# Kernel tuning notes

Measured on AMD Instinct MI355X. Metric: run time of the kernel, lower is better.

Reference implementation:

```python
import jax, jax.numpy as jnp
import numpy as np

B, ES, HS, NL, NOUT, T = 16384, 64, 64, 3, 2, 128


def setup_inputs() -> dict:
    key = jax.random.key(0)
    ks = jax.random.split(key, 9)
    k = 1.0 / np.sqrt(HS)
    u = lambda kk, shape: jax.random.uniform(kk, shape, jnp.float32, -k, k)
    return {
        "agentFutureTrajEnc": jax.random.normal(ks[0], (B, ES), jnp.float32),
        "emb_w": u(ks[1], (ES, ES)),
        "emb_b": u(ks[2], (ES,)),
        "w_ih": u(ks[3], (NL, 3 * HS, ES)),
        "w_hh": u(ks[4], (NL, 3 * HS, HS)),
        "b_ih": u(ks[5], (NL, 3 * HS)),
        "b_hh": u(ks[6], (NL, 3 * HS)),
        "out_w": u(ks[7], (NOUT, HS)),
        "out_b": u(ks[8], (NOUT,)),
        "target_length": T,
        "batch_size": B,
    }


def _gru_cell(x, h, Wi, Wh, bi, bh):
    # PyTorch GRU cell math: gates ordered (r, z, n)
    gi = x @ Wi.T + bi            # (B, 3*hs)
    gh = h @ Wh.T + bh            # (B, 3*hs)
    ir, iz, inn = jnp.split(gi, 3, axis=-1)
    hr, hz, hn = jnp.split(gh, 3, axis=-1)
    r = jax.nn.sigmoid(ir + hr)
    z = jax.nn.sigmoid(iz + hz)
    n = jnp.tanh(inn + r * hn)
    return (1.0 - z) * n + z * h


def reference(agentFutureTrajEnc, emb_w, emb_b, w_ih, w_hh, b_ih, b_hh, out_w, out_b,
              target_length, batch_size):
    nl = w_ih.shape[0]
    # hidden initialized by repeating the encoding across layers: (nl, B, hs)
    h0 = jnp.broadcast_to(agentFutureTrajEnc[None], (nl,) + agentFutureTrajEnc.shape)

    def step(carry, _):
        x, h = carry                      # x: (B, es), h: (nl, B, hs)
        inp = x @ emb_w.T + emb_b         # embedding Linear(es->es)
        new_h = []
        for l in range(nl):               # small fixed layer loop
            hl = _gru_cell(inp, h[l], w_ih[l], w_hh[l], b_ih[l], b_hh[l])
            new_h.append(hl)
            inp = hl
        h = jnp.stack(new_h)              # (nl, B, hs)
        out = inp @ out_w.T + out_b       # (B, nout)
        return (h[-1], h), out            # next input is top-layer hidden

    _, outs = jax.lax.scan(step, (agentFutureTrajEnc, h0), None, length=target_length)
    return jnp.transpose(outs, (1, 0, 2))  # (B, T, nout)
```

## Files before the change

### kernel.cpp

```cpp
#include <hip/hip_runtime.h>


#define ESZ   64
#define HSZ   64
#define TLEN  128
#define NOUTC 2
#define LDW   72
#define TB    (16*LDW)
#define L2E   1.44269504f

typedef _Float16 half8 __attribute__((ext_vector_type(8)));
typedef _Float16 half4 __attribute__((ext_vector_type(4)));
typedef float    floatx4 __attribute__((ext_vector_type(4)));
typedef float    floatx2 __attribute__((ext_vector_type(2)));

#define MFMA(a, b, c) __builtin_amdgcn_mfma_f32_16x16x32_f16((a), (b), (c), 0, 0, 0)

__global__ __launch_bounds__(768, 3) void gru_pipe(
    const float* __restrict__ enc,
    const float* __restrict__ emb_w,
    const float* __restrict__ emb_b,
    const float* __restrict__ w_ih,
    const float* __restrict__ w_hh,
    const float* __restrict__ b_ih,
    const float* __restrict__ b_hh,
    const float* __restrict__ out_w,
    const float* __restrict__ out_b,
    float* __restrict__ out)
{
    __shared__ _Float16 s_hl[3 * 4 * 2 * TB];
    __shared__ float    s_btmp[3 * 64];
    __shared__ int      s_flag[12];

    const int tid  = threadIdx.x;
    const int wave = tid >> 6, lane = tid & 63;
    const int l = wave >> 2, g = wave & 3;
    const int q = lane >> 4, c = lane & 15;
    const int u  = (g << 4) | c;
    const int u4 = (g << 4) | (q << 2);
    const long wgbase = (long)blockIdx.x * 64;

    if (tid < 512) {
        const int row = tid >> 3, k0 = (tid & 7) << 3;
        const int j = row >> 4, rr = row & 15;
        const float* p = enc + (wgbase + row) * ESZ + k0;
        floatx4 s0 = *(const floatx4*)p;
        floatx4 s1 = *(const floatx4*)(p + 4);
        half8 v;
        #pragma unroll
        for (int x = 0; x < 4; ++x) { v[x] = (_Float16)s0[x]; v[4 + x] = (_Float16)s1[x]; }
        #pragma unroll
        for (int ly = 0; ly < 3; ++ly)
            *(half8*)&s_hl[((ly * 4 + j) * 2 + 1) * TB + rr * LDW + k0] = v;
    }
    if (tid < 12) s_flag[tid] = 0;

    auto ldw8s = [&](const float* p, float sc) {
        floatx4 a = *(const floatx4*)p, b = *(const floatx4*)(p + 4);
        half8 v;
        #pragma unroll
        for (int x = 0; x < 4; ++x) { v[x] = (_Float16)(a[x] * sc); v[4 + x] = (_Float16)(b[x] * sc); }
        return v;
    };
    half8 fR[4], fZ[4], fNi[2], fNh[2], fO[2];
    fO[0] = fO[1] = half8{};
    if (l == 0) {
        const float* wi = w_ih;
        const float* wh = w_hh;
        floatx4 aR[4], aZ[4], aN[4];
        #pragma unroll
        for (int x = 0; x < 4; ++x) { aR[x] = {0,0,0,0}; aZ[x] = {0,0,0,0}; aN[x] = {0,0,0,0}; }
        float bR = 0.f, bZ = 0.f, bN = 0.f;
        for (int k4 = 0; k4 < 64; k4 += 4) {
            floatx4 wr4 = *(const floatx4*)(wi + (u) * 64 + k4);
            floatx4 wz4 = *(const floatx4*)(wi + (64 + u) * 64 + k4);
            floatx4 wn4 = *(const floatx4*)(wi + (128 + u) * 64 + k4);
            floatx4 be4 = *(const floatx4*)(emb_b + k4);
            #pragma unroll
            for (int kk = 0; kk < 4; ++kk) {
                const float* er = emb_w + (k4 + kk) * 64;
                floatx4 e0 = *(const floatx4*)(er + q * 8);
                floatx4 e1 = *(const floatx4*)(er + q * 8 + 4);
                floatx4 e2 = *(const floatx4*)(er + 32 + q * 8);
                floatx4 e3 = *(const floatx4*)(er + 32 + q * 8 + 4);
                const float wr = wr4[kk], wz = wz4[kk], wn = wn4[kk];
                aR[0] += wr * e0; aR[1] += wr * e1; aR[2] += wr * e2; aR[3] += wr * e3;
                aZ[0] += wz * e0; aZ[1] += wz * e1; aZ[2] += wz * e2; aZ[3] += wz * e3;
                aN[0] += wn * e0; aN[1] += wn * e1; aN[2] += wn * e2; aN[3] += wn * e3;
                bR += wr * be4[kk]; bZ += wz * be4[kk]; bN += wn * be4[kk];
            }
        }
        #pragma unroll
        for (int x = 0; x < 4; ++x) {
            fR[0][x] = (_Float16)(-L2E * aR[0][x]);   fR[0][4 + x] = (_Float16)(-L2E * aR[1][x]);
            fR[1][x] = (_Float16)(-L2E * aR[2][x]);   fR[1][4 + x] = (_Float16)(-L2E * aR[3][x]);
            fZ[0][x] = (_Float16)(-L2E * aZ[0][x]);   fZ[0][4 + x] = (_Float16)(-L2E * aZ[1][x]);
            fZ[1][x] = (_Float16)(-L2E * aZ[2][x]);   fZ[1][4 + x] = (_Float16)(-L2E * aZ[3][x]);
            fNi[0][x] = (_Float16)(2*L2E * aN[0][x]); fNi[0][4 + x] = (_Float16)(2*L2E * aN[1][x]);
            fNi[1][x] = (_Float16)(2*L2E * aN[2][x]); fNi[1][4 + x] = (_Float16)(2*L2E * aN[3][x]);
        }
        fR[2]  = ldw8s(wh + (u) * 64 + q * 8, -L2E);        fR[3]  = ldw8s(wh + (u) * 64 + 32 + q * 8, -L2E);
        fZ[2]  = ldw8s(wh + (64 + u) * 64 + q * 8, -L2E);   fZ[3]  = ldw8s(wh + (64 + u) * 64 + 32 + q * 8, -L2E);
        fNh[0] = ldw8s(wh + (128 + u) * 64 + q * 8, 2*L2E); fNh[1] = ldw8s(wh + (128 + u) * 64 + 32 + q * 8, 2*L2E);
        if (q == 0) {
            s_btmp[u] = bR; s_btmp[64 + u] = bZ; s_btmp[128 + u] = bN;
        }
        const int oc = (c < NOUTC) ? c : 0;
        fO[0] = ldw8s(out_w + oc * 64 + q * 8, 1.f);
        fO[1] = ldw8s(out_w + oc * 64 + 32 + q * 8, 1.f);
    } else {
        const float* wi = w_ih + l * 3 * HSZ * ESZ;
        const float* wh = w_hh + l * 3 * HSZ * ESZ;
        fR[0]  = ldw8s(wi + (u) * 64 + q * 8, -L2E);        fR[1]  = ldw8s(wi + (u) * 64 + 32 + q * 8, -L2E);
        fR[2]  = ldw8s(wh + (u) * 64 + q * 8, -L2E);        fR[3]  = ldw8s(wh + (u) * 64 + 32 + q * 8, -L2E);
        fZ[0]  = ldw8s(wi + (64 + u) * 64 + q * 8, -L2E);   fZ[1]  = ldw8s(wi + (64 + u) * 64 + 32 + q * 8, -L2E);
        fZ[2]  = ldw8s(wh + (64 + u) * 64 + q * 8, -L2E);   fZ[3]  = ldw8s(wh + (64 + u) * 64 + 32 + q * 8, -L2E);
        fNi[0] = ldw8s(wi + (128 + u) * 64 + q * 8, 2*L2E); fNi[1] = ldw8s(wi + (128 + u) * 64 + 32 + q * 8, 2*L2E);
        fNh[0] = ldw8s(wh + (128 + u) * 64 + q * 8, 2*L2E); fNh[1] = ldw8s(wh + (128 + u) * 64 + 32 + q * 8, 2*L2E);
    }
    __syncthreads();

    floatx4 bR4, bZ4, bNi4, bNh4;
    if (l == 0) {
        #pragma unroll
        for (int i = 0; i < 4; ++i) {
            bR4[i]  = -L2E * (s_btmp[u4 + i] + b_ih[u4 + i] + b_hh[u4 + i]);
            bZ4[i]  = -L2E * (s_btmp[64 + u4 + i] + b_ih[64 + u4 + i] + b_hh[64 + u4 + i]);
            bNi4[i] = 2.f * L2E * (s_btmp[128 + u4 + i] + b_ih[128 + u4 + i]);
            bNh4[i] = 2.f * L2E * b_hh[128 + u4 + i];
        }
    } else {
        const int b0 = l * 192;
        floatx4 bi0 = *(const floatx4*)(b_ih + b0 + u4),       bh0 = *(const floatx4*)(b_hh + b0 + u4);
        floatx4 bi1 = *(const floatx4*)(b_ih + b0 + 64 + u4),  bh1 = *(const floatx4*)(b_hh + b0 + 64 + u4);
        floatx4 bi2 = *(const floatx4*)(b_ih + b0 + 128 + u4), bh2 = *(const floatx4*)(b_hh + b0 + 128 + u4);
        #pragma unroll
        for (int i = 0; i < 4; ++i) {
            bR4[i]  = -L2E * (bi0[i] + bh0[i]);
            bZ4[i]  = -L2E * (bi1[i] + bh1[i]);
            bNi4[i] = 2.f * L2E * bi2[i];
            bNh4[i] = 2.f * L2E * bh2[i];
        }
    }
    const float ob0 = out_b[0], ob1 = out_b[1];

    floatx4 ca0 = *(const floatx4*)(enc + (wgbase + 0 * 16 + c) * 64 + u4);
    floatx4 ca1 = *(const floatx4*)(enc + (wgbase + 1 * 16 + c) * 64 + u4);
    floatx4 ca2 = *(const floatx4*)(enc + (wgbase + 2 * 16 + c) * 64 + u4);
    floatx4 ca3 = *(const floatx4*)(enc + (wgbase + 3 * 16 + c) * 64 + u4);

    const int ar = c * LDW + (q << 3);
    const int fh = l * 4, fx = ((l == 0) ? 2 : (l - 1)) * 4;

    auto iter = [&](const int j, floatx4& carr, const int t) {
        const int parh = (t + 1) & 1, parw = t & 1;
        { volatile const int* f = &s_flag[fh + j]; const int tg = 4 * t; while (*f < tg) {} }
        asm volatile("" ::: "memory");
        const _Float16* hb = s_hl + ((fh + j) * 2 + parh) * TB;
        half8 ah0 = *(const half8*)(hb + ar), ah1 = *(const half8*)(hb + ar + 32);
        floatx4 accr = bR4, accz = bZ4, accni = bNi4, accnh = bNh4;
        accr  = MFMA(fR[2], ah0, accr);   accr  = MFMA(fR[3], ah1, accr);
        accz  = MFMA(fZ[2], ah0, accz);   accz  = MFMA(fZ[3], ah1, accz);
        accnh = MFMA(fNh[0], ah0, accnh); accnh = MFMA(fNh[1], ah1, accnh);
        { volatile const int* f = &s_flag[fx + j]; const int tg = (l == 0) ? 4 * t : 4 * t + 4; while (*f < tg) {} }
        asm volatile("" ::: "memory");
        const _Float16* xb = (l == 0) ? s_hl + ((2 * 4 + j) * 2 + parh) * TB
                                      : s_hl + (((l - 1) * 4 + j) * 2 + parw) * TB;
        half8 bx0 = *(const half8*)(xb + ar), bx1 = *(const half8*)(xb + ar + 32);
        if (l == 0 && g == 0 && t >= 1) {
            floatx4 oa = {ob0, ob1, 0.f, 0.f};
            oa = MFMA(fO[0], bx0, oa);
            oa = MFMA(fO[1], bx1, oa);
            if (q == 0) {
                const long row = wgbase + j * 16 + c;
                *(floatx2*)(out + (row * TLEN + (t - 1)) * NOUTC) = floatx2{oa[0], oa[1]};
            }
        }
        accr  = MFMA(fR[0], bx0, accr);   accr  = MFMA(fR[1], bx1, accr);
        accz  = MFMA(fZ[0], bx0, accz);   accz  = MFMA(fZ[1], bx1, accz);
        accni = MFMA(fNi[0], bx0, accni); accni = MFMA(fNi[1], bx1, accni);
        half4 hv4; floatx4 hnew;
        #pragma unroll
        for (int i = 0; i < 4; ++i) {
            const float r  = __builtin_amdgcn_rcpf(1.f + __builtin_amdgcn_exp2f(accr[i]));
            const float z  = __builtin_amdgcn_rcpf(1.f + __builtin_amdgcn_exp2f(accz[i]));
            const float a  = accni[i] + r * accnh[i];
            const float n  = 1.f - 2.f * __builtin_amdgcn_rcpf(1.f + __builtin_amdgcn_exp2f(a));
            const float hv = n + z * (carr[i] - n);
            hnew[i] = hv; hv4[i] = (_Float16)hv;
        }
        *(half4*)(s_hl + ((fh + j) * 2 + parw) * TB + c * LDW + u4) = hv4;
        carr = hnew;
        asm volatile("s_waitcnt lgkmcnt(0)" ::: "memory");
        if (lane == 0) atomicAdd(&s_flag[fh + j], 1);
    };

    for (int t = 0; t < TLEN; ++t) {
        iter(0, ca0, t); iter(1, ca1, t); iter(2, ca2, t); iter(3, ca3, t);
    }

    if (l == 0 && g == 0) {
        #pragma unroll
        for (int j = 0; j < 4; ++j) {
            { volatile const int* f = &s_flag[2 * 4 + j]; while (*f < 4 * TLEN) {} }
            asm volatile("" ::: "memory");
            const _Float16* xb = s_hl + ((2 * 4 + j) * 2 + 1) * TB;
            half8 bx0 = *(const half8*)(xb + ar), bx1 = *(const half8*)(xb + ar + 32);
            floatx4 oa = {ob0, ob1, 0.f, 0.f};
            oa = MFMA(fO[0], bx0, oa);
            oa = MFMA(fO[1], bx1, oa);
            if (q == 0) {
                const long row = wgbase + j * 16 + c;
                *(floatx2*)(out + (row * TLEN + 127) * NOUTC) = floatx2{oa[0], oa[1]};
            }
        }
    }
}

extern "C" void kernel_launch(void* const* d_in, const int* in_sizes, int n_in,
                              void* d_out, int out_size, void* d_ws, size_t ws_size,
                              hipStream_t stream) {
    (void)in_sizes; (void)n_in; (void)d_ws; (void)ws_size; (void)out_size;
    const int grid = 16384 / 64;
    gru_pipe<<<grid, 768, 0, stream>>>(
        (const float*)d_in[0],
        (const float*)d_in[1],
        (const float*)d_in[2],
        (const float*)d_in[3],
        (const float*)d_in[4],
        (const float*)d_in[5],
        (const float*)d_in[6],
        (const float*)d_in[7],
        (const float*)d_in[8],
        (float*)d_out);
}
```

Measured before the change: 448.3 us.

## Process 32-row batch tiles per pipeline stage and spread output projection across waves

Changes the per-workgroup pipeline from four 16-row tiles to two 32-row tiles. Each wave now issues twice as many independent MFMAs per flag wait, which halves the number of spin-wait and atomic synchronisation points per timestep. The output projection moves out of the critical path: instead of layer-0 wave 0 computing it before its gate MFMAs, it is spread across the four layer-0 waves and issued after the flag release. The cost is higher register pressure and coarser pipeline granularity, which reduces overlap between layers.

```diff
diff --git a/kernel.cpp b/kernel.cpp
--- a/kernel.cpp
+++ b/kernel.cpp
@@ -5,8 +5,9 @@
 #define HSZ   64
 #define TLEN  128
 #define NOUTC 2
+#define NT    2
 #define LDW   72
-#define TB    (16*LDW)
+#define TB32  (32*LDW)
 #define L2E   1.44269504f
 
 typedef _Float16 half8 __attribute__((ext_vector_type(8)));
@@ -28,9 +29,9 @@
     const float* __restrict__ out_b,
     float* __restrict__ out)
 {
-    __shared__ _Float16 s_hl[3 * 4 * 2 * TB];
+    __shared__ _Float16 s_hl[3 * NT * 2 * TB32];
     __shared__ float    s_btmp[3 * 64];
-    __shared__ int      s_flag[12];
+    __shared__ int      s_flag[3 * NT];
 
     const int tid  = threadIdx.x;
     const int wave = tid >> 6, lane = tid & 63;
@@ -42,7 +43,7 @@
 
     if (tid < 512) {
         const int row = tid >> 3, k0 = (tid & 7) << 3;
-        const int j = row >> 4, rr = row & 15;
+        const int j = row >> 5, rr = row & 31;
         const float* p = enc + (wgbase + row) * ESZ + k0;
         floatx4 s0 = *(const floatx4*)p;
         floatx4 s1 = *(const floatx4*)(p + 4);
@@ -51,9 +52,9 @@
         for (int x = 0; x < 4; ++x) { v[x] = (_Float16)s0[x]; v[4 + x] = (_Float16)s1[x]; }
         #pragma unroll
         for (int ly = 0; ly < 3; ++ly)
-            *(half8*)&s_hl[((ly * 4 + j) * 2 + 1) * TB + rr * LDW + k0] = v;
-    }
-    if (tid < 12) s_flag[tid] = 0;
+            *(half8*)&s_hl[((ly * NT + j) * 2 + 1) * TB32 + rr * LDW + k0] = v;
+    }
+    if (tid < 3 * NT) s_flag[tid] = 0;
 
     auto ldw8s = [&](const float* p, float sc) {
         floatx4 a = *(const floatx4*)p, b = *(const floatx4*)(p + 4);
@@ -144,75 +145,107 @@
     }
     const float ob0 = out_b[0], ob1 = out_b[1];
 
-    floatx4 ca0 = *(const floatx4*)(enc + (wgbase + 0 * 16 + c) * 64 + u4);
-    floatx4 ca1 = *(const floatx4*)(enc + (wgbase + 1 * 16 + c) * 64 + u4);
-    floatx4 ca2 = *(const floatx4*)(enc + (wgbase + 2 * 16 + c) * 64 + u4);
-    floatx4 ca3 = *(const floatx4*)(enc + (wgbase + 3 * 16 + c) * 64 + u4);
+    floatx4 ca00 = *(const floatx4*)(enc + (wgbase +  0 + c) * 64 + u4);
+    floatx4 ca01 = *(const floatx4*)(enc + (wgbase + 16 + c) * 64 + u4);
+    floatx4 ca10 = *(const floatx4*)(enc + (wgbase + 32 + c) * 64 + u4);
+    floatx4 ca11 = *(const floatx4*)(enc + (wgbase + 48 + c) * 64 + u4);
 
     const int ar = c * LDW + (q << 3);
-    const int fh = l * 4, fx = ((l == 0) ? 2 : (l - 1)) * 4;
-
-    auto iter = [&](const int j, floatx4& carr, const int t) {
-        const int parh = (t + 1) & 1, parw = t & 1;
+    const int fh = l * NT, fx = ((l == 0) ? 2 : (l - 1)) * NT;
+    const int myj = g >> 1, mys = g & 1;
+
+    auto iter = [&](const int j, floatx4& cs0, floatx4& cs1, const int t,
+                    const int parh, const int parw) {
         { volatile const int* f = &s_flag[fh + j]; const int tg = 4 * t; while (*f < tg) {} }
         asm volatile("" ::: "memory");
-        const _Float16* hb = s_hl + ((fh + j) * 2 + parh) * TB;
-        half8 ah0 = *(const half8*)(hb + ar), ah1 = *(const half8*)(hb + ar + 32);
-        floatx4 accr = bR4, accz = bZ4, accni = bNi4, accnh = bNh4;
-        accr  = MFMA(fR[2], ah0, accr);   accr  = MFMA(fR[3], ah1, accr);
-        accz  = MFMA(fZ[2], ah0, accz);   accz  = MFMA(fZ[3], ah1, accz);
-        accnh = MFMA(fNh[0], ah0, accnh); accnh = MFMA(fNh[1], ah1, accnh);
+        const _Float16* hb = s_hl + ((fh + j) * 2 + parh) * TB32;
+        half8 ah00 = *(const half8*)(hb + ar),             ah01 = *(const half8*)(hb + ar + 32);
+        half8 ah10 = *(const half8*)(hb + ar + 16 * LDW),  ah11 = *(const half8*)(hb + ar + 16 * LDW + 32);
+        floatx4 accr0 = bR4, accz0 = bZ4, accnh0 = bNh4;
+        floatx4 accr1 = bR4, accz1 = bZ4, accnh1 = bNh4;
+        accr0  = MFMA(fR[2], ah00, accr0);   accr0  = MFMA(fR[3], ah01, accr0);
+        accz0  = MFMA(fZ[2], ah00, accz0);   accz0  = MFMA(fZ[3], ah01, accz0);
+        accnh0 = MFMA(fNh[0], ah00, accnh0); accnh0 = MFMA(fNh[1], ah01, accnh0);
+        accr1  = MFMA(fR[2], ah10, accr1);   accr1  = MFMA(fR[3], ah11, accr1);
+        accz1  = MFMA(fZ[2], ah10, accz1);   accz1  = MFMA(fZ[3], ah11, accz1);
+        accnh1 = MFMA(fNh[0], ah10, accnh1); accnh1 = MFMA(fNh[1], ah11, accnh1);
         { volatile const int* f = &s_flag[fx + j]; const int tg = (l == 0) ? 4 * t : 4 * t + 4; while (*f < tg) {} }
         asm volatile("" ::: "memory");
-        const _Float16* xb = (l == 0) ? s_hl + ((2 * 4 + j) * 2 + parh) * TB
-                                      : s_hl + (((l - 1) * 4 + j) * 2 + parw) * TB;
-        half8 bx0 = *(const half8*)(xb + ar), bx1 = *(const half8*)(xb + ar + 32);
-        if (l == 0 && g == 0 && t >= 1) {
-            floatx4 oa = {ob0, ob1, 0.f, 0.f};
-            oa = MFMA(fO[0], bx0, oa);
-            oa = MFMA(fO[1], bx1, oa);
-            if (q == 0) {
-                const long row = wgbase + j * 16 + c;
-                *(floatx2*)(out + (row * TLEN + (t - 1)) * NOUTC) = floatx2{oa[0], oa[1]};
-            }
-        }
-        accr  = MFMA(fR[0], bx0, accr);   accr  = MFMA(fR[1], bx1, accr);
-        accz  = MFMA(fZ[0], bx0, accz);   accz  = MFMA(fZ[1], bx1, accz);
-        accni = MFMA(fNi[0], bx0, accni); accni = MFMA(fNi[1], bx1, accni);
-        half4 hv4; floatx4 hnew;
-        #pragma unroll
-        for (int i = 0; i < 4; ++i) {
-            const float r  = __builtin_amdgcn_rcpf(1.f + __builtin_amdgcn_exp2f(accr[i]));
-            const float z  = __builtin_amdgcn_rcpf(1.f + __builtin_amdgcn_exp2f(accz[i]));
-            const float a  = accni[i] + r * accnh[i];
-            const float n  = 1.f - 2.f * __builtin_amdgcn_rcpf(1.f + __builtin_amdgcn_exp2f(a));
-            const float hv = n + z * (carr[i] - n);
-            hnew[i] = hv; hv4[i] = (_Float16)hv;
-        }
-        *(half4*)(s_hl + ((fh + j) * 2 + parw) * TB + c * LDW + u4) = hv4;
-        carr = hnew;
+        const _Float16* xb = (l == 0) ? s_hl + ((2 * NT + j) * 2 + parh) * TB32
+                                      : s_hl + (((l - 1) * NT + j) * 2 + parw) * TB32;
+        half8 bx00 = *(const half8*)(xb + ar),             bx01 = *(const half8*)(xb + ar + 32);
+        half8 bx10 = *(const half8*)(xb + ar + 16 * LDW),  bx11 = *(const half8*)(xb + ar + 16 * LDW + 32);
+        accr0  = MFMA(fR[0], bx00, accr0);   accr0  = MFMA(fR[1], bx01, accr0);
+        accz0  = MFMA(fZ[0], bx00, accz0);   accz0  = MFMA(fZ[1], bx01, accz0);
+        floatx4 accni0 = bNi4;
+        accni0 = MFMA(fNi[0], bx00, accni0); accni0 = MFMA(fNi[1], bx01, accni0);
+        accr1  = MFMA(fR[0], bx10, accr1);   accr1  = MFMA(fR[1], bx11, accr1);
+        accz1  = MFMA(fZ[0], bx10, accz1);   accz1  = MFMA(fZ[1], bx11, accz1);
+        floatx4 accni1 = bNi4;
+        accni1 = MFMA(fNi[0], bx10, accni1); accni1 = MFMA(fNi[1], bx11, accni1);
+        _Float16* hw = s_hl + ((fh + j) * 2 + parw) * TB32 + c * LDW + u4;
+        {
+            half4 hv4; floatx4 hnew;
+            #pragma unroll
+            for (int i = 0; i < 4; ++i) {
+                const float r  = __builtin_amdgcn_rcpf(1.f + __builtin_amdgcn_exp2f(accr0[i]));
+                const float z  = __builtin_amdgcn_rcpf(1.f + __builtin_amdgcn_exp2f(accz0[i]));
+                const float a  = accni0[i] + r * accnh0[i];
+                const float n  = 1.f - 2.f * __builtin_amdgcn_rcpf(1.f + __builtin_amdgcn_exp2f(a));
+                const float hv = n + z * (cs0[i] - n);
+                hnew[i] = hv; hv4[i] = (_Float16)hv;
+            }
+            *(half4*)hw = hv4;
+            cs0 = hnew;
+        }
+        {
+            half4 hv4; floatx4 hnew;
+            #pragma unroll
+            for (int i = 0; i < 4; ++i) {
+                const float r  = __builtin_amdgcn_rcpf(1.f + __builtin_amdgcn_exp2f(accr1[i]));
+                const float z  = __builtin_amdgcn_rcpf(1.f + __builtin_amdgcn_exp2f(accz1[i]));
+                const float a  = accni1[i] + r * accnh1[i];
+                const float n  = 1.f - 2.f * __builtin_amdgcn_rcpf(1.f + __builtin_amdgcn_exp2f(a));
+                const float hv = n + z * (cs1[i] - n);
+                hnew[i] = hv; hv4[i] = (_Float16)hv;
+            }
+            *(half4*)(hw + 16 * LDW) = hv4;
+            cs1 = hnew;
+        }
         asm volatile("s_waitcnt lgkmcnt(0)" ::: "memory");
         if (lane == 0) atomicAdd(&s_flag[fh + j], 1);
+        if (l == 0 && myj == j && t >= 1) {
+            const half8 ox0 = mys ? bx10 : bx00;
+            const half8 ox1 = mys ? bx11 : bx01;
+            floatx4 oa = {ob0, ob1, 0.f, 0.f};
+            oa = MFMA(fO[0], ox0, oa);
+            oa = MFMA(fO[1], ox1, oa);
+            if (q == 0) {
+                const long row = wgbase + j * 32 + mys * 16 + c;
+                *(floatx2*)(out + (row * TLEN + (t - 1)) * NOUTC) = floatx2{oa[0], oa[1]};
+            }
+        }
     };
 
-    for (int t = 0; t < TLEN; ++t) {
-        iter(0, ca0, t); iter(1, ca1, t); iter(2, ca2, t); iter(3, ca3, t);
-    }
-
-    if (l == 0 && g == 0) {
-        #pragma unroll
-        for (int j = 0; j < 4; ++j) {
-            { volatile const int* f = &s_flag[2 * 4 + j]; while (*f < 4 * TLEN) {} }
-            asm volatile("" ::: "memory");
-            const _Float16* xb = s_hl + ((2 * 4 + j) * 2 + 1) * TB;
-            half8 bx0 = *(const half8*)(xb + ar), bx1 = *(const half8*)(xb + ar + 32);
-            floatx4 oa = {ob0, ob1, 0.f, 0.f};
-            oa = MFMA(fO[0], bx0, oa);
-            oa = MFMA(fO[1], bx1, oa);
-            if (q == 0) {
-                const long row = wgbase + j * 16 + c;
-                *(floatx2*)(out + (row * TLEN + 127) * NOUTC) = floatx2{oa[0], oa[1]};
-            }
+    for (int tt = 0; tt < TLEN; tt += 2) {
+        iter(0, ca00, ca01, tt,     1, 0);
+        iter(1, ca10, ca11, tt,     1, 0);
+        iter(0, ca00, ca01, tt + 1, 0, 1);
+        iter(1, ca10, ca11, tt + 1, 0, 1);
+    }
+
+    if (l == 0) {
+        const int j = myj;
+        { volatile const int* f = &s_flag[2 * NT + j]; while (*f < 4 * TLEN) {} }
+        asm volatile("" ::: "memory");
+        const _Float16* xb = s_hl + ((2 * NT + j) * 2 + 1) * TB32 + mys * 16 * LDW;
+        half8 bx0 = *(const half8*)(xb + ar), bx1 = *(const half8*)(xb + ar + 32);
+        floatx4 oa = {ob0, ob1, 0.f, 0.f};
+        oa = MFMA(fO[0], bx0, oa);
+        oa = MFMA(fO[1], bx1, oa);
+        if (q == 0) {
+            const long row = wgbase + j * 32 + mys * 16 + c;
+            *(floatx2*)(out + (row * TLEN + 127) * NOUTC) = floatx2{oa[0], oa[1]};
         }
     }
 }
```

Measured after the change: 445.9 us. About the same (-0.5%).
